# Kernel optimization log

Hardware: AMD Instinct MI355X
Metric: run time of the kernel (lower is better)

The kernel has to match this reference:

```python
import jax, jax.numpy as jnp
import numpy as np


def setup_inputs() -> dict:
    key = jax.random.key(0)
    kA, kB = jax.random.split(key)
    N = 8192
    A = jax.random.normal(kA, (N, N), dtype=jnp.float32)
    B = jax.random.normal(kB, (N, N), dtype=jnp.float32)
    return {"A": A, "B": B}


def reference(A, B):
    # Kernel computes C[i,j] = sum_{k=i..j} A[i,k] * B[k,j] for i <= j, 0 elsewhere.
    # This equals triu(triu(A) @ triu(B)): k>=i is enforced by triu(A),
    # k<=j by triu(B), and output restricted to the upper triangle.
    C = jnp.triu(A) @ jnp.triu(B)
    return jnp.triu(C)
```

## Files before the change

kernel.cpp:

```cpp
#include <hip/hip_runtime.h>
#include <hip/hip_bf16.h>
#include <stdint.h>

static constexpr int ND = 8192;

typedef __attribute__((ext_vector_type(8))) short bf16x8;
typedef __attribute__((ext_vector_type(4))) float f32x4;

#define GLOBAL_AS __attribute__((address_space(1)))
#define LDS_AS __attribute__((address_space(3)))

__device__ __forceinline__ void gld_lds16(const void* g, void* l) {
    __builtin_amdgcn_global_load_lds((const GLOBAL_AS void*)g, (LDS_AS void*)l, 16, 0, 0);
}

__device__ __forceinline__ unsigned short f2bf(float x) {
    union { float f; uint32_t u; } v; v.f = x;
    uint32_t u = v.u;
    uint32_t r = (u + 0x7fffu + ((u >> 16) & 1u)) >> 16;
    return (unsigned short)r;
}

__global__ void conv_a(const float* __restrict__ A, unsigned short* __restrict__ Aw) {
    uint32_t g = blockIdx.x * 256u + threadIdx.x;
    int i  = (int)(g >> 10);
    int k0 = (int)(g & 1023u) << 3;
    if (k0 + 8 <= (i & ~255)) return;
    const float* src = A + (size_t)i * ND + k0;
    float4 lo = *(const float4*)src;
    float4 hi = *(const float4*)(src + 4);
    float vals[8] = {lo.x, lo.y, lo.z, lo.w, hi.x, hi.y, hi.z, hi.w};
    unsigned short out[8];
#pragma unroll
    for (int e = 0; e < 8; ++e) {
        int k = k0 + e;
        out[e] = (k >= i) ? f2bf(vals[e]) : (unsigned short)0;
    }
    *(uint4*)(Aw + (size_t)i * ND + k0) = *(const uint4*)out;
}

__global__ void conv_bt(const float* __restrict__ B, unsigned short* __restrict__ Bt) {
    __shared__ float tile[64][65];
    int tk = blockIdx.x, tj = blockIdx.y;
    int t = threadIdx.x;
    int k0 = tk * 64, j0 = tj * 64;

    if (k0 > j0 + 63) {
        if (tk >= ((tj >> 2) + 1) * 4) return;
        int jl = t >> 4;
        int kl = (t & 15) * 4;
#pragma unroll
        for (int r = 0; r < 4; ++r) {
            int j = j0 + jl + r * 16;
            *(uint2*)(Bt + (size_t)j * ND + k0 + kl) = make_uint2(0u, 0u);
        }
        return;
    }
    {
        int kl  = t >> 4;
        int jl4 = (t & 15) * 4;
#pragma unroll
        for (int r = 0; r < 4; ++r) {
            int k = k0 + kl + r * 16;
            float4 v = *(const float4*)(B + (size_t)k * ND + j0 + jl4);
            tile[kl + r * 16][jl4 + 0] = v.x;
            tile[kl + r * 16][jl4 + 1] = v.y;
            tile[kl + r * 16][jl4 + 2] = v.z;
            tile[kl + r * 16][jl4 + 3] = v.w;
        }
    }
    __syncthreads();
    {
        int jl  = t >> 4;
        int kl4 = (t & 15) * 4;
#pragma unroll
        for (int r = 0; r < 4; ++r) {
            int j = j0 + jl + r * 16;
            unsigned short o[4];
#pragma unroll
            for (int e = 0; e < 4; ++e) {
                int k = k0 + kl4 + e;
                float v = tile[kl4 + e][jl + r * 16];
                o[e] = (k <= j) ? f2bf(v) : (unsigned short)0;
            }
            *(uint2*)(Bt + (size_t)j * ND + k0 + kl4) = *(const uint2*)o;
        }
    }
}

__global__ __launch_bounds__(256) void zero_lower(float* __restrict__ C) {
    int bid = blockIdx.x;
    int ti = (int)((1.0f + sqrtf(8.0f * (float)bid + 1.0f)) * 0.5f);
    while (ti * (ti + 1) / 2 <= bid) ++ti;
    while (ti * (ti - 1) / 2 > bid) --ti;
    int tj = bid - ti * (ti - 1) / 2;
    if ((ti >> 1) == (tj >> 1)) return;
    int t = threadIdx.x;
    float* base = C + (size_t)(ti * 128) * ND + tj * 128;
    float4 z = {0.f, 0.f, 0.f, 0.f};
#pragma unroll
    for (int it = 0; it < 16; ++it) {
        int row = it * 8 + (t >> 5);
        *(float4*)(base + (size_t)row * ND + (t & 31) * 4) = z;
    }
}

#define BAR() __builtin_amdgcn_s_barrier()
#define WAIT_LGKM0() asm volatile("s_waitcnt lgkmcnt(0)" ::: "memory")
#define WAIT_VM4() asm volatile("s_waitcnt vmcnt(4)" ::: "memory")
#define WAIT_VM0() asm volatile("s_waitcnt vmcnt(0)" ::: "memory")
#define PRIO(x) __builtin_amdgcn_s_setprio(x)

#define LDA(BUF, MH) do { \
    _Pragma("unroll") for (int m_ = 0; m_ < 4; ++m_) \
    _Pragma("unroll") for (int kk_ = 0; kk_ < 2; ++kk_) \
        a_frag[m_][kk_] = *(const bf16x8*)(lds0 + (((BUF)*2 + 0)*2 + (MH))*8192 \
            + (a_lr + m_*16)*64 + (((kk_*4 + khi) ^ lanelo) << 3)); \
} while (0)

#define LDB(BUF, NH) do { \
    _Pragma("unroll") for (int n_ = 0; n_ < 2; ++n_) \
    _Pragma("unroll") for (int kk_ = 0; kk_ < 2; ++kk_) \
        b_frag[NH][n_][kk_] = *(const bf16x8*)(lds0 + (((BUF)*2 + 1)*2 + (NH))*8192 \
            + (b_lr + n_*16)*64 + (((kk_*4 + khi) ^ lanelo) << 3)); \
} while (0)

#define MM(MH, NH) do { \
    _Pragma("unroll") for (int kk_ = 0; kk_ < 2; ++kk_) \
    _Pragma("unroll") for (int m_ = 0; m_ < 4; ++m_) \
    _Pragma("unroll") for (int n_ = 0; n_ < 2; ++n_) \
        acc[(MH)*4 + m_][(NH)*2 + n_] = __builtin_amdgcn_mfma_f32_16x16x32_bf16( \
            a_frag[m_][kk_], b_frag[NH][n_][kk_], acc[(MH)*4 + m_][(NH)*2 + n_], 0, 0, 0); \
} while (0)

__global__ __launch_bounds__(512, 2) void gemm_tri8(const unsigned short* __restrict__ Aw,
                                                    const unsigned short* __restrict__ Bt,
                                                    float* __restrict__ C) {
    int bid = blockIdx.x;
    int s = (int)((sqrtf(8.0f * (float)bid + 1.0f) - 1.0f) * 0.5f);
    while ((s + 1) * (s + 2) / 2 <= bid) ++s;
    while (s * (s + 1) / 2 > bid) --s;
    int tib = bid - s * (s + 1) / 2;
    int tjb = tib + (31 - s);

    __shared__ __align__(16) unsigned short lds[2][2][2][128][64];
    unsigned short* lds0 = &lds[0][0][0][0][0];

    int t = threadIdx.x;
    int lane = t & 63, w = t >> 6;
    int wr = w >> 2, wc = w & 3;
    int lanelo = lane & 7, khi = lane >> 4;
    int a_lr = wr * 64 + (lane & 15);
    int b_lr = wc * 32 + (lane & 15);

    int kstart = tib * 256;
    int nkt = (tjb - tib + 1) * 4;
    int nit = nkt >> 1;

    int srow = w * 8 + (lane >> 3);
    int sg = ((lane & 7) ^ (lane >> 3)) * 8;
    const unsigned short* gA = Aw + (size_t)(tib * 256 + srow) * ND + sg;
    const unsigned short* gB = Bt + (size_t)(tjb * 256 + srow) * ND + sg;
    unsigned short* sdst = lds0 + (w * 512 + lane * 8);

    auto STAGE = [&](int ab, int buf, int h, int ktg) {
        const unsigned short* g = (ab ? gB : gA) + (size_t)(h * 128) * ND + (kstart + ktg * 64);
        unsigned short* l = sdst + ((buf * 2 + ab) * 2 + h) * 8192;
        gld_lds16(g, l);
        gld_lds16(g + (size_t)64 * ND, l + 4096);
    };

    f32x4 acc[8][4];
#pragma unroll
    for (int m = 0; m < 8; ++m)
#pragma unroll
        for (int n = 0; n < 4; ++n) acc[m][n] = (f32x4){0.f, 0.f, 0.f, 0.f};

    bf16x8 a_frag[4][2];
    bf16x8 b_frag[2][2][2];

    STAGE(0, 0, 0, 0); STAGE(1, 0, 0, 0); STAGE(0, 0, 1, 0); STAGE(1, 0, 1, 0);
    STAGE(0, 1, 0, 1); STAGE(1, 1, 0, 1);
    WAIT_VM4();
    BAR();

    for (int I = 0; I < nit; ++I) {
        int k1 = 2 * I + 1, k2 = 2 * I + 2, k3 = 2 * I + 3;
        bool s23 = (k2 < nkt);

        LDA(0, 0); LDB(0, 0);
        STAGE(0, 1, 1, k1);
        BAR(); WAIT_LGKM0(); PRIO(1); MM(0, 0); PRIO(0); BAR();
        LDB(0, 1);
        STAGE(1, 1, 1, k1);
        BAR(); WAIT_LGKM0(); PRIO(1); MM(0, 1); PRIO(0); BAR();
        LDA(0, 1);
        if (s23) STAGE(0, 0, 0, k2);
        BAR(); WAIT_LGKM0(); PRIO(1); MM(1, 0); PRIO(0); BAR();
        if (s23) STAGE(1, 0, 0, k2);
        BAR(); PRIO(1); MM(1, 1); PRIO(0);
        if (s23) { WAIT_VM4(); } else { WAIT_VM0(); }
        BAR();
        LDA(1, 0); LDB(1, 0);
        if (s23) STAGE(0, 0, 1, k2);
        BAR(); WAIT_LGKM0(); PRIO(1); MM(0, 0); PRIO(0); BAR();
        LDB(1, 1);
        if (s23) STAGE(1, 0, 1, k2);
        BAR(); WAIT_LGKM0(); PRIO(1); MM(0, 1); PRIO(0); BAR();
        LDA(1, 1);
        if (s23) STAGE(0, 1, 0, k3);
        BAR(); WAIT_LGKM0(); PRIO(1); MM(1, 0); PRIO(0); BAR();
        if (s23) STAGE(1, 1, 0, k3);
        BAR(); PRIO(1); MM(1, 1); PRIO(0); WAIT_VM4(); BAR();
    }

#pragma unroll
    for (int mh = 0; mh < 2; ++mh)
#pragma unroll
        for (int m = 0; m < 4; ++m)
#pragma unroll
            for (int nh = 0; nh < 2; ++nh)
#pragma unroll
                for (int n = 0; n < 2; ++n) {
                    f32x4 v = acc[mh * 4 + m][nh * 2 + n];
                    int row0 = tib * 256 + mh * 128 + wr * 64 + m * 16 + (lane >> 4) * 4;
                    int col  = tjb * 256 + nh * 128 + wc * 32 + n * 16 + (lane & 15);
#pragma unroll
                    for (int e = 0; e < 4; ++e)
                        C[(size_t)(row0 + e) * ND + col] = v[e];
                }
}

__global__ void tri_naive(const float* __restrict__ A, const float* __restrict__ B,
                          float* __restrict__ C) {
    int j = blockIdx.x * 64 + (threadIdx.x & 63);
    int i = blockIdx.y * 4 + (threadIdx.x >> 6);
    float s = 0.f;
    if (j >= i) {
        for (int k = i; k <= j; ++k) s += A[(size_t)i * ND + k] * B[(size_t)k * ND + j];
        C[(size_t)i * ND + j] = s;
    } else {
        C[(size_t)i * ND + j] = 0.f;
    }
}

extern "C" void kernel_launch(void* const* d_in, const int* in_sizes, int n_in,
                              void* d_out, int out_size, void* d_ws, size_t ws_size,
                              hipStream_t stream) {
    (void)in_sizes; (void)n_in; (void)out_size;
    const float* A = (const float*)d_in[0];
    const float* B = (const float*)d_in[1];
    float* C = (float*)d_out;

    const size_t halfws = (size_t)ND * ND * sizeof(unsigned short);
    if (ws_size >= 2 * halfws) {
        unsigned short* Aw = (unsigned short*)d_ws;
        unsigned short* Bt = (unsigned short*)((char*)d_ws + halfws);

        conv_a<<<dim3(ND * (ND / 8) / 256), dim3(256), 0, stream>>>(A, Aw);
        conv_bt<<<dim3(ND / 64, ND / 64), dim3(256), 0, stream>>>(B, Bt);
        zero_lower<<<dim3(2016), dim3(256), 0, stream>>>(C);
        gemm_tri8<<<dim3(528), dim3(512), 0, stream>>>(Aw, Bt, C);
    } else {
        tri_naive<<<dim3(ND / 64, ND / 4), dim3(256), 0, stream>>>(A, B, C);
    }
}
```

Measured before the change: 345.6 us.

## Split long-K triangular tiles in two with atomic accumulation and LPT ordering

Tiles whose K range is long (diagonal offset at least 16) are split into two half-K jobs that accumulate into C with atomicAdd. The jobs are ordered longest first to balance the 528 unequal triangular tiles across CUs and shrink the tail. This requires a new kernel that zeroes those output tiles before the GEMM runs. It adds an extra zeroing pass and atomic-store traffic on the split tiles.

Measured after the change: 361.8 us. +4.7%, slower.

```diff
diff --git a/kernel.cpp b/kernel.cpp
--- a/kernel.cpp
+++ b/kernel.cpp
@@ -105,6 +105,23 @@
     }
 }
 
+__global__ __launch_bounds__(256) void zero_split(float* __restrict__ C) {
+    int bid = blockIdx.x;
+    int tile = bid >> 2, quad = bid & 3;
+    int d = 31, rem = tile;
+    while (rem >= 32 - d) { rem -= 32 - d; --d; }
+    int tib = rem, tjb = tib + d;
+    int t = threadIdx.x;
+    float* base = C + (size_t)(tib * 256 + (quad >> 1) * 128) * ND
+                    + tjb * 256 + (quad & 1) * 128;
+    float4 z = {0.f, 0.f, 0.f, 0.f};
+#pragma unroll
+    for (int it = 0; it < 16; ++it) {
+        int row = it * 8 + (t >> 5);
+        *(float4*)(base + (size_t)row * ND + (t & 31) * 4) = z;
+    }
+}
+
 #define BAR() __builtin_amdgcn_s_barrier()
 #define WAIT_LGKM0() asm volatile("s_waitcnt lgkmcnt(0)" ::: "memory")
 #define WAIT_VM4() asm volatile("s_waitcnt vmcnt(4)" ::: "memory")
@@ -133,15 +150,44 @@
             a_frag[m_][kk_], b_frag[NH][n_][kk_], acc[(MH)*4 + m_][(NH)*2 + n_], 0, 0, 0); \
 } while (0)
 
+__device__ __forceinline__ void job_map(int bid, int& tib, int& tjb, int& kt0,
+                                        int& nktj, bool& atom) {
+    int rem = bid;
+    for (int v = 64; v >= 4; --v) {
+        if ((v & 1) == 0) {
+            int d = (v >> 1) - 1;
+            if (d >= 16) {
+                int cnt = 2 * (32 - d);
+                if (rem < cnt) {
+                    tib = rem >> 1; tjb = tib + d;
+                    nktj = v; kt0 = (rem & 1) * v; atom = true;
+                    return;
+                }
+                rem -= cnt;
+            }
+        }
+        if ((v & 3) == 0) {
+            int d = (v >> 2) - 1;
+            if (d <= 15) {
+                int cnt = 32 - d;
+                if (rem < cnt) {
+                    tib = rem; tjb = tib + d;
+                    nktj = v; kt0 = 0; atom = false;
+                    return;
+                }
+                rem -= cnt;
+            }
+        }
+    }
+    tib = 0; tjb = 0; kt0 = 0; nktj = 4; atom = false;
+}
+
 __global__ __launch_bounds__(512, 2) void gemm_tri8(const unsigned short* __restrict__ Aw,
                                                     const unsigned short* __restrict__ Bt,
                                                     float* __restrict__ C) {
-    int bid = blockIdx.x;
-    int s = (int)((sqrtf(8.0f * (float)bid + 1.0f) - 1.0f) * 0.5f);
-    while ((s + 1) * (s + 2) / 2 <= bid) ++s;
-    while (s * (s + 1) / 2 > bid) --s;
-    int tib = bid - s * (s + 1) / 2;
-    int tjb = tib + (31 - s);
+    int tib, tjb, kt0j, nkt;
+    bool atom;
+    job_map(blockIdx.x, tib, tjb, kt0j, nkt, atom);
 
     __shared__ __align__(16) unsigned short lds[2][2][2][128][64];
     unsigned short* lds0 = &lds[0][0][0][0][0];
@@ -153,8 +199,7 @@
     int a_lr = wr * 64 + (lane & 15);
     int b_lr = wc * 32 + (lane & 15);
 
-    int kstart = tib * 256;
-    int nkt = (tjb - tib + 1) * 4;
+    int kstart = tib * 256 + kt0j * 64;
     int nit = nkt >> 1;
 
     int srow = w * 8 + (lane >> 3);
@@ -225,9 +270,15 @@
                     f32x4 v = acc[mh * 4 + m][nh * 2 + n];
                     int row0 = tib * 256 + mh * 128 + wr * 64 + m * 16 + (lane >> 4) * 4;
                     int col  = tjb * 256 + nh * 128 + wc * 32 + n * 16 + (lane & 15);
-#pragma unroll
-                    for (int e = 0; e < 4; ++e)
-                        C[(size_t)(row0 + e) * ND + col] = v[e];
+                    if (atom) {
+#pragma unroll
+                        for (int e = 0; e < 4; ++e)
+                            atomicAdd(&C[(size_t)(row0 + e) * ND + col], v[e]);
+                    } else {
+#pragma unroll
+                        for (int e = 0; e < 4; ++e)
+                            C[(size_t)(row0 + e) * ND + col] = v[e];
+                    }
                 }
 }
 
@@ -260,7 +311,8 @@
         conv_a<<<dim3(ND * (ND / 8) / 256), dim3(256), 0, stream>>>(A, Aw);
         conv_bt<<<dim3(ND / 64, ND / 64), dim3(256), 0, stream>>>(B, Bt);
         zero_lower<<<dim3(2016), dim3(256), 0, stream>>>(C);
-        gemm_tri8<<<dim3(528), dim3(512), 0, stream>>>(Aw, Bt, C);
+        zero_split<<<dim3(544), dim3(256), 0, stream>>>(C);
+        gemm_tri8<<<dim3(664), dim3(512), 0, stream>>>(Aw, Bt, C);
     } else {
         tri_naive<<<dim3(ND / 64, ND / 4), dim3(256), 0, stream>>>(A, B, C);
     }
```
